# Kernel tuning notes

Measured on AMD Instinct MI355X. Metric: run time of the kernel, lower is better.

The kernel has to match this reference:

```python
import math
import jax, jax.numpy as jnp
import numpy as np

K = 64            # multiplicity per irrep
NE = 10           # num_elements
N_NODES = 10000
N_EDGES = 100000
AVG_NEIGH = 10.0
EDGE_DIM = 8
LS = [0, 1, 2]    # node/intermediate irreps 64x0e+64x1o+64x2e
LS_OUT = [0, 1]   # output irreps 64x0e+64x1o
INV_SQRT_K = 1.0 / math.sqrt(K)
MIX_NORM = 1.0 / math.sqrt(K * NE)

# ---- real spherical-harmonic Clebsch-Gordan coefficients (small l, exact) ----
def _cg(j1, m1, j2, m2, j3, m3):
    if m1 + m2 != m3 or not (abs(j1 - j2) <= j3 <= j1 + j2):
        return 0.0
    f = math.factorial
    pre = math.sqrt((2 * j3 + 1) * f(j1 + j2 - j3) * f(j1 - j2 + j3) * f(-j1 + j2 + j3) / f(j1 + j2 + j3 + 1))
    pre *= math.sqrt(f(j1 + m1) * f(j1 - m1) * f(j2 + m2) * f(j2 - m2) * f(j3 + m3) * f(j3 - m3))
    s = 0.0
    for k in range(j1 + j2 + j3 + 1):
        d = (j1 + j2 - j3 - k, j1 - m1 - k, j2 + m2 - k, j3 - j2 + m1 + k, j3 - j1 - m2 + k)
        if min(d) < 0:
            continue
        s += (-1) ** k / (f(k) * f(d[0]) * f(d[1]) * f(d[2]) * f(d[3]) * f(d[4]))
    return pre * s

def _u_real(l):
    # complex->real SH change of basis: Y_real = U @ Y_complex
    U = np.zeros((2 * l + 1, 2 * l + 1), dtype=np.complex128)
    U[l, l] = 1.0
    s = 1.0 / math.sqrt(2.0)
    for m in range(1, l + 1):
        U[l + m, l + m] = (-1) ** m * s
        U[l + m, l - m] = s
        U[l - m, l + m] = -1j * (-1) ** m * s
        U[l - m, l - m] = 1j * s
    return U

def real_cg(l1, l2, l3):
    C = np.zeros((2 * l1 + 1, 2 * l2 + 1, 2 * l3 + 1), dtype=np.complex128)
    for m1 in range(-l1, l1 + 1):
        for m2 in range(-l2, l2 + 1):
            m3 = m1 + m2
            if abs(m3) <= l3:
                C[l1 + m1, l2 + m2, l3 + m3] = _cg(l1, m1, l2, m2, l3, m3)
    U1, U2, U3 = _u_real(l1), _u_real(l2), _u_real(l3)
    Cr = np.einsum('ai,bj,ck,ijk->abc', U1, U2, U3.conj(), C)
    return np.ascontiguousarray(Cr.real).astype(np.float32)  # real since l1+l2+l3 even

# parity/triangle allowed paths (l1: edge sph, l2: node in, l3: intermediate) -> 11 paths
EDGE_PATHS = [(l1, l2, l3) for l1 in LS for l2 in LS for l3 in LS
              if abs(l1 - l2) <= l3 <= l1 + l2 and (l1 + l2 + l3) % 2 == 0]
N_EDGE_PATHS = len(EDGE_PATHS)  # 11
DEG2_PATHS = [(0, 0, 0), (1, 1, 0), (2, 2, 0), (0, 1, 1), (1, 2, 1)]
DEG3_PATHS = [(0, 0, 0), (1, 1, 0), (0, 1, 1), (1, 0, 1), (1, 2, 1)]
CG_EDGE = [real_cg(*p) for p in EDGE_PATHS]
CG_D2 = [real_cg(*p) for p in DEG2_PATHS]
CG_D3 = [real_cg(*p) for p in DEG3_PATHS]

def split_irreps(x, ls, mul):
    # ir_mul layout: per irrep a [(2l+1)*mul] flat segment, m index outer
    out, o = [], 0
    for l in ls:
        d = (2 * l + 1) * mul
        out.append(x[:, o:o + d].reshape(x.shape[0], 2 * l + 1, mul))
        o += d
    return out


def setup_inputs() -> dict:
    key = jax.random.key(0)
    ks = jax.random.split(key, 20)
    sender = jax.random.randint(ks[0], (N_EDGES,), 0, N_NODES)
    receiver = jax.random.randint(ks[1], (N_EDGES,), 0, N_NODES)
    indices = jax.random.randint(ks[2], (N_NODES,), 0, NE)
    node_attrs = jax.nn.one_hot(indices, NE, dtype=jnp.float32)
    node_feature_in = jax.random.normal(ks[3], (N_NODES, K * 9), dtype=jnp.float32)
    edge_length_embed = jax.random.normal(ks[4], (N_EDGES, EDGE_DIM), dtype=jnp.float32)
    edge_sph_embed = jax.random.normal(ks[5], (N_EDGES, 9), dtype=jnp.float32)
    W_lin_in = jax.random.normal(ks[6], (3, K, K), dtype=jnp.float32)
    mlp_W0 = jax.random.normal(ks[7], (EDGE_DIM, 32), dtype=jnp.float32) / math.sqrt(EDGE_DIM)
    mlp_b0 = jnp.zeros((32,), jnp.float32)
    mlp_W1 = jax.random.normal(ks[8], (32, 32), dtype=jnp.float32) / math.sqrt(32.0)
    mlp_b1 = jnp.zeros((32,), jnp.float32)
    mlp_W2 = jax.random.normal(ks[9], (32, 32), dtype=jnp.float32) / math.sqrt(32.0)
    mlp_b2 = jnp.zeros((32,), jnp.float32)
    mlp_W3 = jax.random.normal(ks[10], (32, N_EDGE_PATHS * K), dtype=jnp.float32) / math.sqrt(32.0)
    mlp_b3 = jnp.zeros((N_EDGE_PATHS * K,), jnp.float32)
    W_mix = jax.random.normal(ks[11], (3, NE, K, K), dtype=jnp.float32)
    w1 = jax.random.normal(ks[12], (NE, 2, K), dtype=jnp.float32)
    w2 = 0.1 * jax.random.normal(ks[13], (NE, len(DEG2_PATHS), K), dtype=jnp.float32)
    w3 = 0.05 * jax.random.normal(ks[14], (NE, len(DEG3_PATHS), K), dtype=jnp.float32)
    W_out_m = jax.random.normal(ks[15], (2, K, K), dtype=jnp.float32)
    W_out_h = jax.random.normal(ks[16], (2, K, K), dtype=jnp.float32)
    return dict(sender=sender, receiver=receiver, indices=indices, node_attrs=node_attrs,
                node_feature_in=node_feature_in, edge_length_embed=edge_length_embed,
                edge_sph_embed=edge_sph_embed, W_lin_in=W_lin_in,
                mlp_W0=mlp_W0, mlp_b0=mlp_b0, mlp_W1=mlp_W1, mlp_b1=mlp_b1,
                mlp_W2=mlp_W2, mlp_b2=mlp_b2, mlp_W3=mlp_W3, mlp_b3=mlp_b3,
                W_mix=W_mix, w1=w1, w2=w2, w3=w3, W_out_m=W_out_m, W_out_h=W_out_h)


def reference(sender, receiver, indices, node_attrs, node_feature_in,
              edge_length_embed, edge_sph_embed, W_lin_in,
              mlp_W0, mlp_b0, mlp_W1, mlp_b1, mlp_W2, mlp_b2, mlp_W3, mlp_b3,
              W_mix, w1, w2, w3, W_out_m, W_out_h):
    N = node_feature_in.shape[0]
    h1 = split_irreps(node_feature_in, LS, K)  # per-l [N, 2l+1, K]
    # ELinear_h1_2_h1p: per-irrep channel mixing
    h1p = [jnp.einsum('nmc,cd->nmd', h1[l], W_lin_in[l]) * INV_SQRT_K for l in LS]
    # residual radial MLP -> per-edge TP path weights [E, P, K]
    h = jax.nn.silu(edge_length_embed @ mlp_W0 + mlp_b0)
    h = h + jax.nn.silu(h @ mlp_W1 + mlp_b1)
    h = h + jax.nn.silu(h @ mlp_W2 + mlp_b2)
    Rl = (h @ mlp_W3 + mlp_b3).reshape(-1, N_EDGE_PATHS, K)
    sph = split_irreps(edge_sph_embed, LS, 1)  # per-l [E, 2l+1, 1]
    gx = [h1p[l][sender] for l in LS]          # gather sender node features
    # channelwise equivariant tensor product with per-edge radial weights
    msg = [None, None, None]
    for p, (l1, l2, l3) in enumerate(EDGE_PATHS):
        t = jnp.einsum('abd,ea,ebc->edc', jnp.asarray(CG_EDGE[p]), sph[l1][:, :, 0], gx[l2])
        t = t * Rl[:, p, None, :]
        msg[l3] = t if msg[l3] is None else msg[l3] + t
    # scatter-sum messages to receivers, normalized by avg num neighbors
    A = [jax.ops.segment_sum(msg[l], receiver, num_segments=N) / AVG_NEIGH for l in LS]
    # element-conditioned mixing (FCTP with num_elements x 0e attrs)
    Amix = [jnp.einsum('nmc,ne,ecd->nmd', A[l], node_attrs, W_mix[l]) * MIX_NORM for l in LS]
    # symmetric contraction (body order 3) with element-dependent channelwise weights
    w1n, w2n, w3n = w1[indices], w2[indices], w3[indices]
    T2 = [jnp.zeros_like(Amix[L]) for L in LS_OUT]
    for p, (l1, l2, L) in enumerate(DEG2_PATHS):
        t = jnp.einsum('abd,nac,nbc->ndc', jnp.asarray(CG_D2[p]), Amix[l1], Amix[l2])
        T2[L] = T2[L] + w2n[:, p, None, :] * t
    T3 = [jnp.zeros_like(Amix[L]) for L in LS_OUT]
    for q, (Lp, l3, L) in enumerate(DEG3_PATHS):
        t = jnp.einsum('abd,nac,nbc->ndc', jnp.asarray(CG_D3[q]), T2[Lp], Amix[l3])
        T3[L] = T3[L] + w3n[:, q, None, :] * t
    B = [w1n[:, L, None, :] * Amix[L] + T2[L] + T3[L] for L in LS_OUT]
    # node_feature_out = ELinear_h1_2_h2(h1) + ELinear_m2_2_h2(B)
    out = []
    for L in LS_OUT:
        y = jnp.einsum('nmc,cd->nmd', h1[L], W_out_h[L]) * INV_SQRT_K
        y = y + jnp.einsum('nmc,cd->nmd', B[L], W_out_m[L]) * INV_SQRT_K
        out.append(y.reshape(N, -1))
    return jnp.concatenate(out, axis=1)  # [N, 4K] = [N, 256]
```

## Files before the change

kernel.cpp:

```cpp
#include <hip/hip_runtime.h>
#include <math.h>

#define NNODES 10000
#define NEDGES 100000

struct Cplx { double re, im; };

constexpr double cfact(int n){ double r=1.0; for(int i=2;i<=n;++i) r*=i; return r; }

constexpr double csqrt_(double x){
  if (x<=0.0) return 0.0;
  double g = x<1.0 ? 1.0 : x;
  for (int it=0; it<64; ++it){ double ng = 0.5*(g + x/g); if (ng==g) break; g = ng; }
  return g;
}

constexpr double cg_coeff(int j1,int m1,int j2,int m2,int j3,int m3){
  if (m1+m2!=m3) return 0.0;
  int lo = j1>j2 ? j1-j2 : j2-j1;
  if (j3<lo || j3>j1+j2) return 0.0;
  if (m1<-j1||m1>j1||m2<-j2||m2>j2||m3<-j3||m3>j3) return 0.0;
  double pre = csqrt_((2.0*j3+1.0)*cfact(j1+j2-j3)*cfact(j1-j2+j3)*cfact(-j1+j2+j3)/cfact(j1+j2+j3+1));
  pre *= csqrt_(cfact(j1+m1)*cfact(j1-m1)*cfact(j2+m2)*cfact(j2-m2)*cfact(j3+m3)*cfact(j3-m3));
  double s = 0.0;
  for (int k=0;k<=j1+j2+j3;++k){
    int d0=j1+j2-j3-k, d1=j1-m1-k, d2=j2+m2-k, d3=j3-j2+m1+k, d4=j3-j1-m2+k;
    if (d0<0||d1<0||d2<0||d3<0||d4<0) continue;
    double term = 1.0/(cfact(k)*cfact(d0)*cfact(d1)*cfact(d2)*cfact(d3)*cfact(d4));
    s += (k&1) ? -term : term;
  }
  return pre*s;
}

constexpr Cplx uent(int l,int a,int i){
  const double s = 0.70710678118654752440;
  int ma = a - l;
  if (ma==0) { if (i==l) return Cplx{1.0,0.0}; return Cplx{0.0,0.0}; }
  if (ma>0){
    int m = ma; double sg = (m&1) ? -1.0 : 1.0;
    if (i==l+m) return Cplx{sg*s, 0.0};
    if (i==l-m) return Cplx{s, 0.0};
    return Cplx{0.0,0.0};
  }
  int m = -ma; double sg = (m&1) ? -1.0 : 1.0;
  if (i==l+m) return Cplx{0.0, -sg*s};
  if (i==l-m) return Cplx{0.0, s};
  return Cplx{0.0,0.0};
}

constexpr double real_cg_entry(int l1,int l2,int l3,int a,int b,int c){
  double acc = 0.0;
  int ii0 = a, ii1 = 2*l1-a;
  int jj0 = b, jj1 = 2*l2-b;
  for (int x=0;x<2;++x){
    int i = (x==0)? ii0 : ii1;
    if (x==1 && ii1==ii0) break;
    Cplx u1 = uent(l1,a,i); if (u1.re==0.0 && u1.im==0.0) continue;
    for (int y=0;y<2;++y){
      int j = (y==0)? jj0 : jj1;
      if (y==1 && jj1==jj0) break;
      Cplx u2 = uent(l2,b,j); if (u2.re==0.0 && u2.im==0.0) continue;
      int k = (i-l1)+(j-l2)+l3;
      if (k<0 || k>2*l3) continue;
      Cplx u3 = uent(l3,c,k); if (u3.re==0.0 && u3.im==0.0) continue;
      double cg = cg_coeff(l1,i-l1,l2,j-l2,l3,k-l3);
      if (cg==0.0) continue;
      double pr = u1.re*u2.re - u1.im*u2.im;
      double pi = u1.re*u2.im + u1.im*u2.re;
      acc += (pr*u3.re + pi*u3.im) * cg;
    }
  }
  return acc;
}

struct CGT { float v[5][5][5]; };
constexpr CGT make_cg(int l1,int l2,int l3){
  CGT t{};
  for (int a=0;a<2*l1+1;++a)
    for (int b=0;b<2*l2+1;++b)
      for (int c=0;c<2*l3+1;++c)
        t.v[a][b][c] = (float)real_cg_entry(l1,l2,l3,a,b,c);
  return t;
}

__device__ __forceinline__ float silu_(float x){ return x / (1.0f + __expf(-x)); }

union H16 { _Float16 h; unsigned short u; };
__device__ __forceinline__ unsigned short f2h(float x){ H16 c; c.h = (_Float16)x; return c.u; }
__device__ __forceinline__ float h2f(unsigned short u){ H16 c; c.u = u; return (float)c.h; }

template<int L1,int L2,int L3>
__device__ __forceinline__ void tp_accum(const float* sp, const float* g, float rl, float* msg){
  constexpr CGT T = make_cg(L1,L2,L3);
  constexpr int NA = 2*L1+1, NB = 2*L2+1, ND = 2*L3+1;
  float t[ND];
#pragma unroll
  for (int d=0; d<ND; ++d) t[d] = 0.f;
#pragma unroll
  for (int b=0;b<NB;++b){
#pragma unroll
    for (int d=0; d<ND; ++d){
      float u = 0.f; bool any = false;
#pragma unroll
      for (int a=0;a<NA;++a){
        const float cg = T.v[a][b][d];
        if (cg != 0.f){ u = fmaf(cg, sp[a], u); any = true; }
      }
      if (any) t[d] = fmaf(u, g[b], t[d]);
    }
  }
#pragma unroll
  for (int d=0;d<ND;++d) msg[d] = fmaf(rl, t[d], msg[d]);
}

template<int L1,int L2,int L3>
__device__ __forceinline__ void sc_accum(const float* X, const float* Y, float w, float* out){
  constexpr CGT T = make_cg(L1,L2,L3);
  constexpr int NA = 2*L1+1, NB = 2*L2+1, ND = 2*L3+1;
#pragma unroll
  for (int d=0;d<ND;++d){
    float s = 0.f;
#pragma unroll
    for (int a=0;a<NA;++a){
#pragma unroll
      for (int b=0;b<NB;++b){
        const float cg = T.v[a][b][d];
        if (cg != 0.f) s = fmaf(cg*X[a], Y[b], s);
      }
    }
    out[d] = fmaf(w, s, out[d]);
  }
}

__global__ void __launch_bounds__(64) k_lin_in(const float* __restrict__ h1,
                                               const float* __restrict__ W,
                                               float* __restrict__ h1p,
                                               int* __restrict__ deg){
  const int n = blockIdx.x;
  const int d = threadIdx.x;
  if (d == 0) deg[n] = 0;
  const float* row = h1 + (long)n*576;
  float acc[9];
#pragma unroll
  for (int i=0;i<9;++i) acc[i] = 0.f;
  for (int c=0;c<64;++c){
    const float w0 = W[c*64 + d];
    const float w1 = W[4096 + c*64 + d];
    const float w2 = W[8192 + c*64 + d];
    acc[0] = fmaf(row[c], w0, acc[0]);
#pragma unroll
    for (int m=0;m<3;++m) acc[1+m] = fmaf(row[64+m*64+c], w1, acc[1+m]);
#pragma unroll
    for (int m=0;m<5;++m) acc[4+m] = fmaf(row[256+m*64+c], w2, acc[4+m]);
  }
  float* o = h1p + (long)n*576;
  o[d] = acc[0]*0.125f;
#pragma unroll
  for (int m=0;m<3;++m) o[64+m*64+d] = acc[1+m]*0.125f;
#pragma unroll
  for (int m=0;m<5;++m) o[256+m*64+d] = acc[4+m]*0.125f;
}

__global__ void __launch_bounds__(256) k_mlp(const float* __restrict__ ele,
                                             const float* __restrict__ W0, const float* __restrict__ b0,
                                             const float* __restrict__ W1, const float* __restrict__ b1,
                                             const float* __restrict__ W2, const float* __restrict__ b2,
                                             float* __restrict__ hmlp){
  const int e = blockIdx.x*256 + threadIdx.x;
  if (e >= NEDGES) return;
  float x[8];
#pragma unroll
  for (int i=0;i<8;++i) x[i] = ele[(long)e*8 + i];
  float h[32];
#pragma unroll
  for (int d=0;d<32;++d){
    float acc = b0[d];
#pragma unroll
    for (int i=0;i<8;++i) acc = fmaf(x[i], W0[i*32+d], acc);
    h[d] = silu_(acc);
  }
#pragma unroll
  for (int L=0; L<2; ++L){
    const float* Wl = L ? W2 : W1;
    const float* bl = L ? b2 : b1;
    float acc[32];
#pragma unroll
    for (int d=0;d<32;++d) acc[d] = bl[d];
    for (int j=0;j<32;++j){
      const float hj = h[j];
#pragma unroll
      for (int d=0;d<32;++d) acc[d] = fmaf(hj, Wl[j*32+d], acc[d]);
    }
#pragma unroll
    for (int d=0;d<32;++d) h[d] += silu_(acc[d]);
  }
  float* o = hmlp + (long)e*32;
#pragma unroll
  for (int d=0;d<32;++d) o[d] = h[d];
}

__global__ void __launch_bounds__(256) k_hist(const int* __restrict__ receiver, int* __restrict__ deg){
  const int e = blockIdx.x*256 + threadIdx.x;
  if (e < NEDGES) atomicAdd(&deg[receiver[e]], 1);
}

__global__ void __launch_bounds__(256) k_scan(const int* __restrict__ deg,
                                              int* __restrict__ rowptr,
                                              int* __restrict__ cursor){
  __shared__ int sums[256];
  const int t = threadIdx.x;
  const int CH = 40;
  const int base = t*CH;
  int s = 0;
  for (int i=0;i<CH;++i){ int idx = base+i; if (idx < NNODES) s += deg[idx]; }
  sums[t] = s; __syncthreads();
  for (int off=1; off<256; off<<=1){
    int v = (t>=off) ? sums[t-off] : 0;
    __syncthreads();
    sums[t] += v;
    __syncthreads();
  }
  int run = (t==0) ? 0 : sums[t-1];
  for (int i=0;i<CH;++i){
    int idx = base+i;
    if (idx < NNODES){ rowptr[idx] = run; cursor[idx] = run; run += deg[idx]; }
  }
  if (t==255) rowptr[NNODES] = sums[255];
}

__global__ void __launch_bounds__(256) k_fill(const int* __restrict__ receiver,
                                              int* __restrict__ cursor,
                                              int* __restrict__ eidx){
  const int e = blockIdx.x*256 + threadIdx.x;
  if (e < NEDGES){
    int pos = atomicAdd(&cursor[receiver[e]], 1);
    eidx[pos] = e;
  }
}

__global__ void __launch_bounds__(256, 2) k_edge_all(const int* __restrict__ sender,
                                             const float* __restrict__ hmlp,
                                             const float* __restrict__ sph,
                                             const float* __restrict__ h1p,
                                             const float* __restrict__ W3, const float* __restrict__ b3,
                                             unsigned short* __restrict__ msg16){
  __shared__ float sps[4][72];
  const int wid  = threadIdx.x >> 6;
  const int lane = threadIdx.x & 63;
  const int ubase = __builtin_amdgcn_readfirstlane((blockIdx.x*4 + wid) * 8);

  sps[wid][lane] = sph[(long)ubase*9 + lane];
  if (lane < 8) sps[wid][64+lane] = sph[(long)ubase*9 + 64 + lane];

  int sidx[8];
#pragma unroll
  for (int e=0;e<8;++e) sidx[e] = sender[ubase+e];

  float g[8][9];
#pragma unroll
  for (int e=0;e<8;++e){
    const float* hp = h1p + (long)sidx[e]*576;
#pragma unroll
    for (int i=0;i<9;++i) g[e][i] = hp[i*64+lane];
  }
#pragma unroll
  for (int e=0;e<8;++e)
#pragma unroll
    for (int i=0;i<9;++i) asm volatile("" : "+v"(g[e][i]));

  const float* hu = hmlp + (long)ubase*32;

  float rl[11][8];
#pragma unroll
  for (int p=0;p<11;++p){
    const float bb = b3[p*64+lane];
#pragma unroll
    for (int e=0;e<8;++e) rl[p][e] = bb;
  }
  for (int jb=0;jb<32;jb+=4){
    float w3v[4][11];
#pragma unroll
    for (int jj=0;jj<4;++jj)
#pragma unroll
      for (int p=0;p<11;++p)
        w3v[jj][p] = W3[(jb+jj)*704 + p*64 + lane];
#pragma unroll
    for (int e=0;e<8;++e){
#pragma unroll
      for (int jj=0;jj<4;++jj){
        const float hj = hu[e*32 + jb + jj];
#pragma unroll
        for (int p=0;p<11;++p) rl[p][e] = fmaf(hj, w3v[jj][p], rl[p][e]);
      }
    }
  }

#pragma unroll
  for (int e=0;e<8;++e){
    const float* sp = &sps[wid][e*9];
    const size_t mb = (size_t)(ubase+e)*576;
    float m0[1] = {0.f};
    float m1[3] = {0.f,0.f,0.f};
    float m2[5] = {0.f,0.f,0.f,0.f,0.f};
    tp_accum<0,0,0>(sp+0, &g[e][0], rl[0][e],  m0);
    tp_accum<0,1,1>(sp+0, &g[e][1], rl[1][e],  m1);
    tp_accum<0,2,2>(sp+0, &g[e][4], rl[2][e],  m2);
    tp_accum<1,0,1>(sp+1, &g[e][0], rl[3][e],  m1);
    tp_accum<1,1,0>(sp+1, &g[e][1], rl[4][e],  m0);
    tp_accum<1,1,2>(sp+1, &g[e][1], rl[5][e],  m2);
    tp_accum<1,2,1>(sp+1, &g[e][4], rl[6][e],  m1);
    tp_accum<2,0,2>(sp+4, &g[e][0], rl[7][e],  m2);
    tp_accum<2,1,1>(sp+4, &g[e][1], rl[8][e],  m1);
    tp_accum<2,2,0>(sp+4, &g[e][4], rl[9][e],  m0);
    tp_accum<2,2,2>(sp+4, &g[e][4], rl[10][e], m2);
    msg16[mb + lane] = f2h(m0[0]);
#pragma unroll
    for (int m=0;m<3;++m) msg16[mb + (1+m)*64 + lane] = f2h(m1[m]);
#pragma unroll
    for (int m=0;m<5;++m) msg16[mb + (4+m)*64 + lane] = f2h(m2[m]);
  }
}

__global__ void __launch_bounds__(256) k_node_w(const int* __restrict__ indices,
                                             const float* __restrict__ h1,
                                             const int* __restrict__ rowptr,
                                             const int* __restrict__ eidx,
                                             const unsigned short* __restrict__ msg16,
                                             const float* __restrict__ Wmix,
                                             const float* __restrict__ w1,
                                             const float* __restrict__ w2,
                                             const float* __restrict__ w3,
                                             const float* __restrict__ Wom,
                                             const float* __restrict__ Woh,
                                             float* __restrict__ out){
  __shared__ float S[4][9][64];
  __shared__ float Bb[4][4][64];
  const int wid  = threadIdx.x >> 6;
  const int lane = threadIdx.x & 63;
  const int n = blockIdx.x*4 + wid;
  const int e = __builtin_amdgcn_readfirstlane(indices[n]);

  {
    const int start = rowptr[n], end = rowptr[n+1];
    float A[9];
#pragma unroll
    for (int i=0;i<9;++i) A[i] = 0.f;
    for (int q=start; q<end; ++q){
      const int ed = eidx[q];
      const unsigned short* mp = msg16 + (size_t)ed*576;
#pragma unroll
      for (int i=0;i<9;++i) A[i] += h2f(mp[i*64+lane]);
    }
#pragma unroll
    for (int i=0;i<9;++i) S[wid][i][lane] = A[i];
  }

  float ax[9];
#pragma unroll
  for (int i=0;i<9;++i) ax[i] = 0.f;
  {
    const float* Wm0 = Wmix + (size_t)(0*10 + e)*4096;
    const float* Wm1 = Wmix + (size_t)(1*10 + e)*4096;
    const float* Wm2 = Wmix + (size_t)(2*10 + e)*4096;
    for (int c=0;c<64;++c){
      const float wv0 = Wm0[c*64+lane];
      const float wv1 = Wm1[c*64+lane];
      const float wv2 = Wm2[c*64+lane];
      ax[0] = fmaf(S[wid][0][c], wv0, ax[0]);
#pragma unroll
      for (int m=0;m<3;++m) ax[1+m] = fmaf(S[wid][1+m][c], wv1, ax[1+m]);
#pragma unroll
      for (int m=0;m<5;++m) ax[4+m] = fmaf(S[wid][4+m][c], wv2, ax[4+m]);
    }
  }
#pragma unroll
  for (int i=0;i<9;++i) ax[i] *= 0.0039528470752104741f;

  const float* amix0 = ax;
  const float* amix1 = ax+1;
  const float* amix2 = ax+4;
  float w2n[5], w3n[5];
#pragma unroll
  for (int p=0;p<5;++p){
    w2n[p] = w2[(size_t)(e*5+p)*64 + lane];
    w3n[p] = w3[(size_t)(e*5+p)*64 + lane];
  }
  float t20[1] = {0.f}, t21[3] = {0.f,0.f,0.f};
  sc_accum<0,0,0>(amix0, amix0, w2n[0], t20);
  sc_accum<1,1,0>(amix1, amix1, w2n[1], t20);
  sc_accum<2,2,0>(amix2, amix2, w2n[2], t20);
  sc_accum<0,1,1>(amix0, amix1, w2n[3], t21);
  sc_accum<1,2,1>(amix1, amix2, w2n[4], t21);
  float t30[1] = {0.f}, t31[3] = {0.f,0.f,0.f};
  sc_accum<0,0,0>(t20, amix0, w3n[0], t30);
  sc_accum<1,1,0>(t21, amix1, w3n[1], t30);
  sc_accum<0,1,1>(t20, amix1, w3n[2], t31);
  sc_accum<1,0,1>(t21, amix0, w3n[3], t31);
  sc_accum<1,2,1>(t21, amix2, w3n[4], t31);

  const float w1_0 = w1[(size_t)(e*2+0)*64 + lane];
  const float w1_1 = w1[(size_t)(e*2+1)*64 + lane];
  Bb[wid][0][lane] = fmaf(w1_0, amix0[0], t20[0] + t30[0]);
#pragma unroll
  for (int m=0;m<3;++m) Bb[wid][1+m][lane] = fmaf(w1_1, amix1[m], t21[m] + t31[m]);

  {
    const float* hrow = h1 + (long)n*576;
#pragma unroll
    for (int r=0;r<9;++r) S[wid][r][lane] = hrow[r*64 + lane];
  }

  float o[4];
#pragma unroll
  for (int i=0;i<4;++i) o[i] = 0.f;
  for (int c=0;c<64;++c){
    const float wh0 = Woh[c*64+lane];
    const float wh1 = Woh[4096 + c*64+lane];
    const float wm0 = Wom[c*64+lane];
    const float wm1 = Wom[4096 + c*64+lane];
    o[0] = fmaf(S[wid][0][c], wh0, o[0]);
    o[0] = fmaf(Bb[wid][0][c], wm0, o[0]);
#pragma unroll
    for (int m=0;m<3;++m){
      o[1+m] = fmaf(S[wid][1+m][c], wh1, o[1+m]);
      o[1+m] = fmaf(Bb[wid][1+m][c], wm1, o[1+m]);
    }
  }
  float* orow = out + (long)n*256;
  orow[lane] = o[0]*0.125f;
#pragma unroll
  for (int m=0;m<3;++m) orow[64+m*64+lane] = o[1+m]*0.125f;
}

extern "C" void kernel_launch(void* const* d_in, const int* in_sizes, int n_in,
                              void* d_out, int out_size, void* d_ws, size_t ws_size,
                              hipStream_t stream){
  const int*   sender   = (const int*)  d_in[0];
  const int*   receiver = (const int*)  d_in[1];
  const int*   indices  = (const int*)  d_in[2];
  const float* node_feat= (const float*)d_in[4];
  const float* ele      = (const float*)d_in[5];
  const float* sph      = (const float*)d_in[6];
  const float* W_lin    = (const float*)d_in[7];
  const float* W0 = (const float*)d_in[8],  *b0 = (const float*)d_in[9];
  const float* W1 = (const float*)d_in[10], *b1 = (const float*)d_in[11];
  const float* W2 = (const float*)d_in[12], *b2 = (const float*)d_in[13];
  const float* W3 = (const float*)d_in[14], *b3 = (const float*)d_in[15];
  const float* Wmix = (const float*)d_in[16];
  const float* w1 = (const float*)d_in[17];
  const float* w2 = (const float*)d_in[18];
  const float* w3 = (const float*)d_in[19];
  const float* Wom = (const float*)d_in[20];
  const float* Woh = (const float*)d_in[21];
  float* out = (float*)d_out;

  char* ws = (char*)d_ws;
  const size_t OFF_H1P  = 0;
  const size_t OFF_HMLP = OFF_H1P  + (size_t)NNODES*576*4;
  const size_t OFF_MSG  = OFF_HMLP + (size_t)NEDGES*32*4;
  const size_t OFF_DEG  = OFF_MSG  + (size_t)NEDGES*576*2;
  const size_t OFF_ROW  = OFF_DEG  + 40960;
  const size_t OFF_CUR  = OFF_ROW  + 40960;
  const size_t OFF_EIDX = OFF_CUR  + 40960;

  float* h1p  = (float*)(ws + OFF_H1P);
  float* hmlp = (float*)(ws + OFF_HMLP);
  unsigned short* msg16 = (unsigned short*)(ws + OFF_MSG);
  int* deg    = (int*)(ws + OFF_DEG);
  int* rowptr = (int*)(ws + OFF_ROW);
  int* cursor = (int*)(ws + OFF_CUR);
  int* eidx   = (int*)(ws + OFF_EIDX);

  k_lin_in<<<NNODES, 64, 0, stream>>>(node_feat, W_lin, h1p, deg);
  k_mlp<<<(NEDGES+255)/256, 256, 0, stream>>>(ele, W0,b0,W1,b1,W2,b2, hmlp);
  k_hist<<<(NEDGES+255)/256, 256, 0, stream>>>(receiver, deg);
  k_scan<<<1, 256, 0, stream>>>(deg, rowptr, cursor);
  k_fill<<<(NEDGES+255)/256, 256, 0, stream>>>(receiver, cursor, eidx);
  k_edge_all<<<NEDGES/32, 256, 0, stream>>>(sender, hmlp, sph, h1p, W3, b3, msg16);
  k_node_w<<<NNODES/4, 256, 0, stream>>>(indices, node_feat, rowptr, eidx, msg16,
                                         Wmix, w1, w2, w3, Wom, Woh, out);
}
```

Measured before the change: 266.8 us.

## Precompute per-edge CG-SH products and write receiver-sorted packed fp16 messages

The prep kernel now also folds each edge's spherical harmonics into the Clebsch-Gordan coefficients and stores a 120-float U tensor per edge. A new edge kernel uses U for the tensor product and writes packed half2 messages directly at the edge's receiver-sorted position, found with an atomic cursor. A new node kernel then reads the messages contiguously instead of going through an edge-index list. The aim is to cut CG arithmetic in the edge kernel and the gather indirection in the node kernel, at the cost of extra global traffic for U and padded messages. The new path runs only if the workspace is large enough; otherwise the old path runs, and there prep writes U past the eidx buffer.

```diff
diff --git a/kernel.cpp b/kernel.cpp
--- a/kernel.cpp
+++ b/kernel.cpp
@@ -88,6 +88,50 @@
 union H16 { _Float16 h; unsigned short u; };
 __device__ __forceinline__ unsigned short f2h(float x){ H16 c; c.h = (_Float16)x; return c.u; }
 __device__ __forceinline__ float h2f(unsigned short u){ H16 c; c.u = u; return (float)c.h; }
+__device__ __forceinline__ unsigned int pack2(float a, float b){
+  H16 x, y; x.h = (_Float16)a; y.h = (_Float16)b;
+  return ((unsigned int)y.u << 16) | x.u;
+}
+
+template<int L1,int L2,int L3>
+__device__ __forceinline__ void u_comp(const float* sp, float* dst){
+  constexpr CGT T = make_cg(L1,L2,L3);
+  constexpr int NA = 2*L1+1, NB = 2*L2+1, ND = 2*L3+1;
+#pragma unroll
+  for (int b=0;b<NB;++b){
+#pragma unroll
+    for (int d=0;d<ND;++d){
+      float u = 0.f; bool any = false;
+#pragma unroll
+      for (int a=0;a<NA;++a){
+        const float cg = T.v[a][b][d];
+        if (cg != 0.f){ u = fmaf(cg, sp[a], u); any = true; }
+      }
+      if (any) dst[b*ND+d] = u;
+    }
+  }
+}
+
+template<int L1,int L2,int L3>
+__device__ __forceinline__ void tp_u(const float* Ue, const float* g, float rl, float* msg){
+  constexpr CGT T = make_cg(L1,L2,L3);
+  constexpr int NA = 2*L1+1, NB = 2*L2+1, ND = 2*L3+1;
+  float t[ND];
+#pragma unroll
+  for (int d=0;d<ND;++d) t[d] = 0.f;
+#pragma unroll
+  for (int b=0;b<NB;++b){
+#pragma unroll
+    for (int d=0;d<ND;++d){
+      bool any = false;
+#pragma unroll
+      for (int a=0;a<NA;++a) if (T.v[a][b][d] != 0.f) any = true;
+      if (any) t[d] = fmaf(Ue[b*ND+d], g[b], t[d]);
+    }
+  }
+#pragma unroll
+  for (int d=0;d<ND;++d) msg[d] = fmaf(rl, t[d], msg[d]);
+}
 
 template<int L1,int L2,int L3>
 __device__ __forceinline__ void tp_accum(const float* sp, const float* g, float rl, float* msg){
@@ -161,11 +205,13 @@
   for (int m=0;m<5;++m) o[256+m*64+d] = acc[4+m]*0.125f;
 }
 
-__global__ void __launch_bounds__(256) k_mlp(const float* __restrict__ ele,
-                                             const float* __restrict__ W0, const float* __restrict__ b0,
-                                             const float* __restrict__ W1, const float* __restrict__ b1,
-                                             const float* __restrict__ W2, const float* __restrict__ b2,
-                                             float* __restrict__ hmlp){
+__global__ void __launch_bounds__(256) k_prep(const float* __restrict__ ele,
+                                              const float* __restrict__ sph,
+                                              const float* __restrict__ W0, const float* __restrict__ b0,
+                                              const float* __restrict__ W1, const float* __restrict__ b1,
+                                              const float* __restrict__ W2, const float* __restrict__ b2,
+                                              float* __restrict__ hmlp,
+                                              float* __restrict__ U){
   const int e = blockIdx.x*256 + threadIdx.x;
   if (e >= NEDGES) return;
   float x[8];
@@ -197,6 +243,22 @@
   float* o = hmlp + (long)e*32;
 #pragma unroll
   for (int d=0;d<32;++d) o[d] = h[d];
+
+  float sp[9];
+#pragma unroll
+  for (int i=0;i<9;++i) sp[i] = sph[(long)e*9 + i];
+  float* Up = U + (size_t)e*120;
+  u_comp<0,0,0>(sp+0, Up+0);
+  u_comp<0,1,1>(sp+0, Up+1);
+  u_comp<0,2,2>(sp+0, Up+10);
+  u_comp<1,0,1>(sp+1, Up+35);
+  u_comp<1,1,0>(sp+1, Up+38);
+  u_comp<1,1,2>(sp+1, Up+41);
+  u_comp<1,2,1>(sp+1, Up+56);
+  u_comp<2,0,2>(sp+4, Up+71);
+  u_comp<2,1,1>(sp+4, Up+76);
+  u_comp<2,2,0>(sp+4, Up+85);
+  u_comp<2,2,2>(sp+4, Up+90);
 }
 
 __global__ void __launch_bounds__(256) k_hist(const int* __restrict__ receiver, int* __restrict__ deg){
@@ -228,6 +290,13 @@
   if (t==255) rowptr[NNODES] = sums[255];
 }
 
+__global__ void __launch_bounds__(256) k_fill_pos(const int* __restrict__ receiver,
+                                                  int* __restrict__ cursor,
+                                                  int* __restrict__ epos){
+  const int e = blockIdx.x*256 + threadIdx.x;
+  if (e < NEDGES) epos[e] = atomicAdd(&cursor[receiver[e]], 1);
+}
+
 __global__ void __launch_bounds__(256) k_fill(const int* __restrict__ receiver,
                                               int* __restrict__ cursor,
                                               int* __restrict__ eidx){
@@ -236,6 +305,202 @@
     int pos = atomicAdd(&cursor[receiver[e]], 1);
     eidx[pos] = e;
   }
+}
+
+__global__ void __launch_bounds__(256) k_edge_u(const int* __restrict__ sender,
+                                             const int* __restrict__ epos,
+                                             const float* __restrict__ hmlp,
+                                             const float* __restrict__ U,
+                                             const float* __restrict__ h1p,
+                                             const float* __restrict__ W3, const float* __restrict__ b3,
+                                             unsigned int* __restrict__ msg){
+  const int wid  = threadIdx.x >> 6;
+  const int lane = threadIdx.x & 63;
+  const int ubase = __builtin_amdgcn_readfirstlane((blockIdx.x*4 + wid) * 8);
+
+  int sidx[8], pos[8];
+#pragma unroll
+  for (int e=0;e<8;++e){ sidx[e] = sender[ubase+e]; pos[e] = epos[ubase+e]; }
+
+  float g[8][9];
+#pragma unroll
+  for (int e=0;e<8;++e){
+    const float* hp = h1p + (long)sidx[e]*576;
+#pragma unroll
+    for (int i=0;i<9;++i) g[e][i] = hp[i*64+lane];
+  }
+#pragma unroll
+  for (int e=0;e<8;++e)
+#pragma unroll
+    for (int i=0;i<9;++i) asm volatile("" : "+v"(g[e][i]));
+
+  const float* hu = hmlp + (long)ubase*32;
+
+  float rl[11][8];
+#pragma unroll
+  for (int p=0;p<11;++p){
+    const float bb = b3[p*64+lane];
+#pragma unroll
+    for (int e=0;e<8;++e) rl[p][e] = bb;
+  }
+  for (int jb=0;jb<32;jb+=4){
+    float w3v[4][11];
+#pragma unroll
+    for (int jj=0;jj<4;++jj)
+#pragma unroll
+      for (int p=0;p<11;++p)
+        w3v[jj][p] = W3[(jb+jj)*704 + p*64 + lane];
+#pragma unroll
+    for (int e=0;e<8;++e){
+#pragma unroll
+      for (int jj=0;jj<4;++jj){
+        const float hj = hu[e*32 + jb + jj];
+#pragma unroll
+        for (int p=0;p<11;++p) rl[p][e] = fmaf(hj, w3v[jj][p], rl[p][e]);
+      }
+    }
+  }
+
+#pragma unroll
+  for (int e=0;e<8;++e){
+    const float* Ue = U + (size_t)(ubase+e)*120;
+    float m0[1] = {0.f};
+    float m1[3] = {0.f,0.f,0.f};
+    float m2[5] = {0.f,0.f,0.f,0.f,0.f};
+    tp_u<0,0,0>(Ue+0,  &g[e][0], rl[0][e],  m0);
+    tp_u<0,1,1>(Ue+1,  &g[e][1], rl[1][e],  m1);
+    tp_u<0,2,2>(Ue+10, &g[e][4], rl[2][e],  m2);
+    tp_u<1,0,1>(Ue+35, &g[e][0], rl[3][e],  m1);
+    tp_u<1,1,0>(Ue+38, &g[e][1], rl[4][e],  m0);
+    tp_u<1,1,2>(Ue+41, &g[e][1], rl[5][e],  m2);
+    tp_u<1,2,1>(Ue+56, &g[e][4], rl[6][e],  m1);
+    tp_u<2,0,2>(Ue+71, &g[e][0], rl[7][e],  m2);
+    tp_u<2,1,1>(Ue+76, &g[e][1], rl[8][e],  m1);
+    tp_u<2,2,0>(Ue+85, &g[e][4], rl[9][e],  m0);
+    tp_u<2,2,2>(Ue+90, &g[e][4], rl[10][e], m2);
+    unsigned int pk[5];
+    pk[0] = pack2(m0[0], m1[0]);
+    pk[1] = pack2(m1[1], m1[2]);
+    pk[2] = pack2(m2[0], m2[1]);
+    pk[3] = pack2(m2[2], m2[3]);
+    pk[4] = pack2(m2[4], 0.f);
+    unsigned int* mp = msg + (size_t)pos[e]*320;
+#pragma unroll
+    for (int k=0;k<5;++k) mp[k*64 + lane] = pk[k];
+  }
+}
+
+__global__ void __launch_bounds__(256) k_node_c(const int* __restrict__ indices,
+                                             const float* __restrict__ h1,
+                                             const int* __restrict__ rowptr,
+                                             const unsigned int* __restrict__ msg,
+                                             const float* __restrict__ Wmix,
+                                             const float* __restrict__ w1,
+                                             const float* __restrict__ w2,
+                                             const float* __restrict__ w3,
+                                             const float* __restrict__ Wom,
+                                             const float* __restrict__ Woh,
+                                             float* __restrict__ out){
+  __shared__ float S[4][9][64];
+  __shared__ float Bb[4][4][64];
+  const int wid  = threadIdx.x >> 6;
+  const int lane = threadIdx.x & 63;
+  const int n = blockIdx.x*4 + wid;
+  const int e = __builtin_amdgcn_readfirstlane(indices[n]);
+
+  {
+    const int start = rowptr[n], end = rowptr[n+1];
+    float A[9];
+#pragma unroll
+    for (int i=0;i<9;++i) A[i] = 0.f;
+    for (int q=start; q<end; ++q){
+      const unsigned int* mp = msg + (size_t)q*320;
+#pragma unroll
+      for (int k=0;k<5;++k){
+        const unsigned int v = mp[k*64 + lane];
+        A[2*k] += h2f((unsigned short)(v & 0xffff));
+        if (2*k+1 < 9) A[2*k+1] += h2f((unsigned short)(v >> 16));
+      }
+    }
+#pragma unroll
+    for (int i=0;i<9;++i) S[wid][i][lane] = A[i];
+  }
+
+  float ax[9];
+#pragma unroll
+  for (int i=0;i<9;++i) ax[i] = 0.f;
+  {
+    const float* Wm0 = Wmix + (size_t)(0*10 + e)*4096;
+    const float* Wm1 = Wmix + (size_t)(1*10 + e)*4096;
+    const float* Wm2 = Wmix + (size_t)(2*10 + e)*4096;
+    for (int c=0;c<64;++c){
+      const float wv0 = Wm0[c*64+lane];
+      const float wv1 = Wm1[c*64+lane];
+      const float wv2 = Wm2[c*64+lane];
+      ax[0] = fmaf(S[wid][0][c], wv0, ax[0]);
+#pragma unroll
+      for (int m=0;m<3;++m) ax[1+m] = fmaf(S[wid][1+m][c], wv1, ax[1+m]);
+#pragma unroll
+      for (int m=0;m<5;++m) ax[4+m] = fmaf(S[wid][4+m][c], wv2, ax[4+m]);
+    }
+  }
+#pragma unroll
+  for (int i=0;i<9;++i) ax[i] *= 0.0039528470752104741f;
+
+  const float* amix0 = ax;
+  const float* amix1 = ax+1;
+  const float* amix2 = ax+4;
+  float w2n[5], w3n[5];
+#pragma unroll
+  for (int p=0;p<5;++p){
+    w2n[p] = w2[(size_t)(e*5+p)*64 + lane];
+    w3n[p] = w3[(size_t)(e*5+p)*64 + lane];
+  }
+  float t20[1] = {0.f}, t21[3] = {0.f,0.f,0.f};
+  sc_accum<0,0,0>(amix0, amix0, w2n[0], t20);
+  sc_accum<1,1,0>(amix1, amix1, w2n[1], t20);
+  sc_accum<2,2,0>(amix2, amix2, w2n[2], t20);
+  sc_accum<0,1,1>(amix0, amix1, w2n[3], t21);
+  sc_accum<1,2,1>(amix1, amix2, w2n[4], t21);
+  float t30[1] = {0.f}, t31[3] = {0.f,0.f,0.f};
+  sc_accum<0,0,0>(t20, amix0, w3n[0], t30);
+  sc_accum<1,1,0>(t21, amix1, w3n[1], t30);
+  sc_accum<0,1,1>(t20, amix1, w3n[2], t31);
+  sc_accum<1,0,1>(t21, amix0, w3n[3], t31);
+  sc_accum<1,2,1>(t21, amix2, w3n[4], t31);
+
+  const float w1_0 = w1[(size_t)(e*2+0)*64 + lane];
+  const float w1_1 = w1[(size_t)(e*2+1)*64 + lane];
+  Bb[wid][0][lane] = fmaf(w1_0, amix0[0], t20[0] + t30[0]);
+#pragma unroll
+  for (int m=0;m<3;++m) Bb[wid][1+m][lane] = fmaf(w1_1, amix1[m], t21[m] + t31[m]);
+
+  {
+    const float* hrow = h1 + (long)n*576;
+#pragma unroll
+    for (int r=0;r<9;++r) S[wid][r][lane] = hrow[r*64 + lane];
+  }
+
+  float o[4];
+#pragma unroll
+  for (int i=0;i<4;++i) o[i] = 0.f;
+  for (int c=0;c<64;++c){
+    const float wh0 = Woh[c*64+lane];
+    const float wh1 = Woh[4096 + c*64+lane];
+    const float wm0 = Wom[c*64+lane];
+    const float wm1 = Wom[4096 + c*64+lane];
+    o[0] = fmaf(S[wid][0][c], wh0, o[0]);
+    o[0] = fmaf(Bb[wid][0][c], wm0, o[0]);
+#pragma unroll
+    for (int m=0;m<3;++m){
+      o[1+m] = fmaf(S[wid][1+m][c], wh1, o[1+m]);
+      o[1+m] = fmaf(Bb[wid][1+m][c], wm1, o[1+m]);
+    }
+  }
+  float* orow = out + (long)n*256;
+  orow[lane] = o[0]*0.125f;
+#pragma unroll
+  for (int m=0;m<3;++m) orow[64+m*64+lane] = o[1+m]*0.125f;
 }
 
 __global__ void __launch_bounds__(256, 2) k_edge_all(const int* __restrict__ sender,
@@ -455,28 +720,58 @@
   float* out = (float*)d_out;
 
   char* ws = (char*)d_ws;
+
   const size_t OFF_H1P  = 0;
   const size_t OFF_HMLP = OFF_H1P  + (size_t)NNODES*576*4;
-  const size_t OFF_MSG  = OFF_HMLP + (size_t)NEDGES*32*4;
-  const size_t OFF_DEG  = OFF_MSG  + (size_t)NEDGES*576*2;
+  const size_t OFF_U    = OFF_HMLP + (size_t)NEDGES*32*4;
+  const size_t OFF_MSG  = OFF_U    + (size_t)NEDGES*120*4;
+  const size_t OFF_DEG  = OFF_MSG  + (size_t)NEDGES*320*4;
   const size_t OFF_ROW  = OFF_DEG  + 40960;
   const size_t OFF_CUR  = OFF_ROW  + 40960;
-  const size_t OFF_EIDX = OFF_CUR  + 40960;
-
-  float* h1p  = (float*)(ws + OFF_H1P);
-  float* hmlp = (float*)(ws + OFF_HMLP);
-  unsigned short* msg16 = (unsigned short*)(ws + OFF_MSG);
-  int* deg    = (int*)(ws + OFF_DEG);
-  int* rowptr = (int*)(ws + OFF_ROW);
-  int* cursor = (int*)(ws + OFF_CUR);
-  int* eidx   = (int*)(ws + OFF_EIDX);
-
-  k_lin_in<<<NNODES, 64, 0, stream>>>(node_feat, W_lin, h1p, deg);
-  k_mlp<<<(NEDGES+255)/256, 256, 0, stream>>>(ele, W0,b0,W1,b1,W2,b2, hmlp);
-  k_hist<<<(NEDGES+255)/256, 256, 0, stream>>>(receiver, deg);
-  k_scan<<<1, 256, 0, stream>>>(deg, rowptr, cursor);
-  k_fill<<<(NEDGES+255)/256, 256, 0, stream>>>(receiver, cursor, eidx);
-  k_edge_all<<<NEDGES/32, 256, 0, stream>>>(sender, hmlp, sph, h1p, W3, b3, msg16);
-  k_node_w<<<NNODES/4, 256, 0, stream>>>(indices, node_feat, rowptr, eidx, msg16,
-                                         Wmix, w1, w2, w3, Wom, Woh, out);
-}
+  const size_t OFF_EPOS = OFF_CUR  + 40960;
+  const size_t FAST_NEED = OFF_EPOS + (size_t)NEDGES*4 + 4096;
+
+  if (ws_size >= FAST_NEED){
+    float* h1p  = (float*)(ws + OFF_H1P);
+    float* hmlp = (float*)(ws + OFF_HMLP);
+    float* U    = (float*)(ws + OFF_U);
+    unsigned int* msg = (unsigned int*)(ws + OFF_MSG);
+    int* deg    = (int*)(ws + OFF_DEG);
+    int* rowptr = (int*)(ws + OFF_ROW);
+    int* cursor = (int*)(ws + OFF_CUR);
+    int* epos   = (int*)(ws + OFF_EPOS);
+
+    k_lin_in<<<NNODES, 64, 0, stream>>>(node_feat, W_lin, h1p, deg);
+    k_prep<<<(NEDGES+255)/256, 256, 0, stream>>>(ele, sph, W0,b0,W1,b1,W2,b2, hmlp, U);
+    k_hist<<<(NEDGES+255)/256, 256, 0, stream>>>(receiver, deg);
+    k_scan<<<1, 256, 0, stream>>>(deg, rowptr, cursor);
+    k_fill_pos<<<(NEDGES+255)/256, 256, 0, stream>>>(receiver, cursor, epos);
+    k_edge_u<<<NEDGES/32, 256, 0, stream>>>(sender, epos, hmlp, U, h1p, W3, b3, msg);
+    k_node_c<<<NNODES/4, 256, 0, stream>>>(indices, node_feat, rowptr, msg,
+                                           Wmix, w1, w2, w3, Wom, Woh, out);
+  } else {
+    const size_t F_H1P  = 0;
+    const size_t F_HMLP = F_H1P  + (size_t)NNODES*576*4;
+    const size_t F_MSG  = F_HMLP + (size_t)NEDGES*32*4;
+    const size_t F_DEG  = F_MSG  + (size_t)NEDGES*576*2;
+    const size_t F_ROW  = F_DEG  + 40960;
+    const size_t F_CUR  = F_ROW  + 40960;
+    const size_t F_EIDX = F_CUR  + 40960;
+    float* h1p  = (float*)(ws + F_H1P);
+    float* hmlp = (float*)(ws + F_HMLP);
+    unsigned short* msg16 = (unsigned short*)(ws + F_MSG);
+    int* deg    = (int*)(ws + F_DEG);
+    int* rowptr = (int*)(ws + F_ROW);
+    int* cursor = (int*)(ws + F_CUR);
+    int* eidx   = (int*)(ws + F_EIDX);
+
+    k_lin_in<<<NNODES, 64, 0, stream>>>(node_feat, W_lin, h1p, deg);
+    k_prep<<<(NEDGES+255)/256, 256, 0, stream>>>(ele, sph, W0,b0,W1,b1,W2,b2, hmlp, (float*)(ws + F_EIDX + (size_t)NEDGES*4));
+    k_hist<<<(NEDGES+255)/256, 256, 0, stream>>>(receiver, deg);
+    k_scan<<<1, 256, 0, stream>>>(deg, rowptr, cursor);
+    k_fill<<<(NEDGES+255)/256, 256, 0, stream>>>(receiver, cursor, eidx);
+    k_edge_all<<<NEDGES/32, 256, 0, stream>>>(sender, hmlp, sph, h1p, W3, b3, msg16);
+    k_node_w<<<NNODES/4, 256, 0, stream>>>(indices, node_feat, rowptr, eidx, msg16,
+                                           Wmix, w1, w2, w3, Wom, Woh, out);
+  }
+}
```

After: 343.6 us. 28.8% more time.

## Pack edge math into float2, write messages in receiver-sorted order, pack fp16 pairs

Applied to the files above, without the earlier changes.

The edge kernel now handles two edges at once using float2 vector arithmetic, so the compiler can emit packed FMA instructions. Messages are written straight to their receiver-sorted slot (the fill kernel records each edge's position instead of an edge-index list). Message storage uses 32-bit words that hold two fp16 values, padded to 10 halves per channel. The node gather then reads contiguous rows without the indirection, at the cost of scattered writes in the edge kernel, slightly larger message storage, and dropping the occupancy hint of 2 from launch bounds.

```diff
diff --git a/kernel.cpp b/kernel.cpp
--- a/kernel.cpp
+++ b/kernel.cpp
@@ -3,6 +3,8 @@
 
 #define NNODES 10000
 #define NEDGES 100000
+
+typedef float v2f __attribute__((ext_vector_type(2)));
 
 struct Cplx { double re, im; };
 
@@ -86,31 +88,35 @@
 __device__ __forceinline__ float silu_(float x){ return x / (1.0f + __expf(-x)); }
 
 union H16 { _Float16 h; unsigned short u; };
-__device__ __forceinline__ unsigned short f2h(float x){ H16 c; c.h = (_Float16)x; return c.u; }
 __device__ __forceinline__ float h2f(unsigned short u){ H16 c; c.u = u; return (float)c.h; }
+__device__ __forceinline__ unsigned int pack2(float a, float b){
+  H16 x, y; x.h = (_Float16)a; y.h = (_Float16)b;
+  return ((unsigned int)y.u << 16) | x.u;
+}
+__device__ __forceinline__ v2f make2(float s){ v2f r; r.x = s; r.y = s; return r; }
 
 template<int L1,int L2,int L3>
-__device__ __forceinline__ void tp_accum(const float* sp, const float* g, float rl, float* msg){
+__device__ __forceinline__ void tp_pk(const v2f* sp, const v2f* g, v2f rl, v2f* msg){
   constexpr CGT T = make_cg(L1,L2,L3);
   constexpr int NA = 2*L1+1, NB = 2*L2+1, ND = 2*L3+1;
-  float t[ND];
-#pragma unroll
-  for (int d=0; d<ND; ++d) t[d] = 0.f;
+  v2f t[ND];
+#pragma unroll
+  for (int d=0;d<ND;++d) t[d] = make2(0.f);
 #pragma unroll
   for (int b=0;b<NB;++b){
 #pragma unroll
-    for (int d=0; d<ND; ++d){
-      float u = 0.f; bool any = false;
+    for (int d=0;d<ND;++d){
+      v2f u = make2(0.f); bool any = false;
 #pragma unroll
       for (int a=0;a<NA;++a){
         const float cg = T.v[a][b][d];
-        if (cg != 0.f){ u = fmaf(cg, sp[a], u); any = true; }
+        if (cg != 0.f){ u = cg*sp[a] + u; any = true; }
       }
-      if (any) t[d] = fmaf(u, g[b], t[d]);
-    }
-  }
-#pragma unroll
-  for (int d=0;d<ND;++d) msg[d] = fmaf(rl, t[d], msg[d]);
+      if (any) t[d] = u*g[b] + t[d];
+    }
+  }
+#pragma unroll
+  for (int d=0;d<ND;++d) msg[d] = rl*t[d] + msg[d];
 }
 
 template<int L1,int L2,int L3>
@@ -228,54 +234,61 @@
   if (t==255) rowptr[NNODES] = sums[255];
 }
 
-__global__ void __launch_bounds__(256) k_fill(const int* __restrict__ receiver,
-                                              int* __restrict__ cursor,
-                                              int* __restrict__ eidx){
+__global__ void __launch_bounds__(256) k_fill_pos(const int* __restrict__ receiver,
+                                                  int* __restrict__ cursor,
+                                                  int* __restrict__ epos){
   const int e = blockIdx.x*256 + threadIdx.x;
-  if (e < NEDGES){
-    int pos = atomicAdd(&cursor[receiver[e]], 1);
-    eidx[pos] = e;
-  }
-}
-
-__global__ void __launch_bounds__(256, 2) k_edge_all(const int* __restrict__ sender,
+  if (e < NEDGES) epos[e] = atomicAdd(&cursor[receiver[e]], 1);
+}
+
+__global__ void __launch_bounds__(256) k_edge_pk(const int* __restrict__ sender,
+                                             const int* __restrict__ epos,
                                              const float* __restrict__ hmlp,
                                              const float* __restrict__ sph,
                                              const float* __restrict__ h1p,
                                              const float* __restrict__ W3, const float* __restrict__ b3,
-                                             unsigned short* __restrict__ msg16){
+                                             unsigned int* __restrict__ msg){
   __shared__ float sps[4][72];
   const int wid  = threadIdx.x >> 6;
   const int lane = threadIdx.x & 63;
   const int ubase = __builtin_amdgcn_readfirstlane((blockIdx.x*4 + wid) * 8);
 
-  sps[wid][lane] = sph[(long)ubase*9 + lane];
-  if (lane < 8) sps[wid][64+lane] = sph[(long)ubase*9 + 64 + lane];
-
-  int sidx[8];
-#pragma unroll
-  for (int e=0;e<8;++e) sidx[e] = sender[ubase+e];
-
-  float g[8][9];
-#pragma unroll
-  for (int e=0;e<8;++e){
-    const float* hp = h1p + (long)sidx[e]*576;
-#pragma unroll
-    for (int i=0;i<9;++i) g[e][i] = hp[i*64+lane];
-  }
-#pragma unroll
-  for (int e=0;e<8;++e)
-#pragma unroll
-    for (int i=0;i<9;++i) asm volatile("" : "+v"(g[e][i]));
+  {
+    const int idx = lane;
+    const int e = idx/9, a = idx - 9*e;
+    sps[wid][a*8 + e] = sph[(long)ubase*9 + idx];
+  }
+  if (lane < 8){
+    const int idx = 64 + lane;
+    const int e = idx/9, a = idx - 9*e;
+    sps[wid][a*8 + e] = sph[(long)ubase*9 + idx];
+  }
+
+  int sidx[8], pos[8];
+#pragma unroll
+  for (int e=0;e<8;++e){ sidx[e] = sender[ubase+e]; pos[e] = epos[ubase+e]; }
+
+  v2f g2[4][9];
+#pragma unroll
+  for (int q=0;q<4;++q){
+    const float* hp0 = h1p + (long)sidx[2*q]  *576;
+    const float* hp1 = h1p + (long)sidx[2*q+1]*576;
+#pragma unroll
+    for (int i=0;i<9;++i){ g2[q][i].x = hp0[i*64+lane]; g2[q][i].y = hp1[i*64+lane]; }
+  }
+#pragma unroll
+  for (int q=0;q<4;++q)
+#pragma unroll
+    for (int i=0;i<9;++i) asm volatile("" : "+v"(g2[q][i]));
 
   const float* hu = hmlp + (long)ubase*32;
 
-  float rl[11][8];
+  v2f rl2[11][4];
 #pragma unroll
   for (int p=0;p<11;++p){
     const float bb = b3[p*64+lane];
 #pragma unroll
-    for (int e=0;e<8;++e) rl[p][e] = bb;
+    for (int q=0;q<4;++q) rl2[p][q] = make2(bb);
   }
   for (int jb=0;jb<32;jb+=4){
     float w3v[4][11];
@@ -285,47 +298,64 @@
       for (int p=0;p<11;++p)
         w3v[jj][p] = W3[(jb+jj)*704 + p*64 + lane];
 #pragma unroll
-    for (int e=0;e<8;++e){
+    for (int q=0;q<4;++q){
 #pragma unroll
       for (int jj=0;jj<4;++jj){
-        const float hj = hu[e*32 + jb + jj];
-#pragma unroll
-        for (int p=0;p<11;++p) rl[p][e] = fmaf(hj, w3v[jj][p], rl[p][e]);
+        v2f h2; h2.x = hu[(2*q)*32 + jb + jj]; h2.y = hu[(2*q+1)*32 + jb + jj];
+#pragma unroll
+        for (int p=0;p<11;++p) rl2[p][q] = h2*w3v[jj][p] + rl2[p][q];
       }
     }
   }
 
 #pragma unroll
-  for (int e=0;e<8;++e){
-    const float* sp = &sps[wid][e*9];
-    const size_t mb = (size_t)(ubase+e)*576;
-    float m0[1] = {0.f};
-    float m1[3] = {0.f,0.f,0.f};
-    float m2[5] = {0.f,0.f,0.f,0.f,0.f};
-    tp_accum<0,0,0>(sp+0, &g[e][0], rl[0][e],  m0);
-    tp_accum<0,1,1>(sp+0, &g[e][1], rl[1][e],  m1);
-    tp_accum<0,2,2>(sp+0, &g[e][4], rl[2][e],  m2);
-    tp_accum<1,0,1>(sp+1, &g[e][0], rl[3][e],  m1);
-    tp_accum<1,1,0>(sp+1, &g[e][1], rl[4][e],  m0);
-    tp_accum<1,1,2>(sp+1, &g[e][1], rl[5][e],  m2);
-    tp_accum<1,2,1>(sp+1, &g[e][4], rl[6][e],  m1);
-    tp_accum<2,0,2>(sp+4, &g[e][0], rl[7][e],  m2);
-    tp_accum<2,1,1>(sp+4, &g[e][1], rl[8][e],  m1);
-    tp_accum<2,2,0>(sp+4, &g[e][4], rl[9][e],  m0);
-    tp_accum<2,2,2>(sp+4, &g[e][4], rl[10][e], m2);
-    msg16[mb + lane] = f2h(m0[0]);
-#pragma unroll
-    for (int m=0;m<3;++m) msg16[mb + (1+m)*64 + lane] = f2h(m1[m]);
-#pragma unroll
-    for (int m=0;m<5;++m) msg16[mb + (4+m)*64 + lane] = f2h(m2[m]);
-  }
-}
-
-__global__ void __launch_bounds__(256) k_node_w(const int* __restrict__ indices,
+  for (int q=0;q<4;++q){
+    v2f sp2[9];
+#pragma unroll
+    for (int a=0;a<9;++a) sp2[a] = *(const v2f*)&sps[wid][a*8 + 2*q];
+    v2f m0[1]; m0[0] = make2(0.f);
+    v2f m1[3]; m1[0]=m1[1]=m1[2]=make2(0.f);
+    v2f m2[5]; m2[0]=m2[1]=m2[2]=m2[3]=m2[4]=make2(0.f);
+    tp_pk<0,0,0>(sp2+0, &g2[q][0], rl2[0][q],  m0);
+    tp_pk<0,1,1>(sp2+0, &g2[q][1], rl2[1][q],  m1);
+    tp_pk<0,2,2>(sp2+0, &g2[q][4], rl2[2][q],  m2);
+    tp_pk<1,0,1>(sp2+1, &g2[q][0], rl2[3][q],  m1);
+    tp_pk<1,1,0>(sp2+1, &g2[q][1], rl2[4][q],  m0);
+    tp_pk<1,1,2>(sp2+1, &g2[q][1], rl2[5][q],  m2);
+    tp_pk<1,2,1>(sp2+1, &g2[q][4], rl2[6][q],  m1);
+    tp_pk<2,0,2>(sp2+4, &g2[q][0], rl2[7][q],  m2);
+    tp_pk<2,1,1>(sp2+4, &g2[q][1], rl2[8][q],  m1);
+    tp_pk<2,2,0>(sp2+4, &g2[q][4], rl2[9][q],  m0);
+    tp_pk<2,2,2>(sp2+4, &g2[q][4], rl2[10][q], m2);
+    {
+      unsigned int pk[5];
+      pk[0] = pack2(m0[0].x, m1[0].x);
+      pk[1] = pack2(m1[1].x, m1[2].x);
+      pk[2] = pack2(m2[0].x, m2[1].x);
+      pk[3] = pack2(m2[2].x, m2[3].x);
+      pk[4] = pack2(m2[4].x, 0.f);
+      unsigned int* mp = msg + (size_t)pos[2*q]*320;
+#pragma unroll
+      for (int k=0;k<5;++k) mp[k*64 + lane] = pk[k];
+    }
+    {
+      unsigned int pk[5];
+      pk[0] = pack2(m0[0].y, m1[0].y);
+      pk[1] = pack2(m1[1].y, m1[2].y);
+      pk[2] = pack2(m2[0].y, m2[1].y);
+      pk[3] = pack2(m2[2].y, m2[3].y);
+      pk[4] = pack2(m2[4].y, 0.f);
+      unsigned int* mp = msg + (size_t)pos[2*q+1]*320;
+#pragma unroll
+      for (int k=0;k<5;++k) mp[k*64 + lane] = pk[k];
+    }
+  }
+}
+
+__global__ void __launch_bounds__(256) k_node_c(const int* __restrict__ indices,
                                              const float* __restrict__ h1,
                                              const int* __restrict__ rowptr,
-                                             const int* __restrict__ eidx,
-                                             const unsigned short* __restrict__ msg16,
+                                             const unsigned int* __restrict__ msg,
                                              const float* __restrict__ Wmix,
                                              const float* __restrict__ w1,
                                              const float* __restrict__ w2,
@@ -346,10 +376,13 @@
 #pragma unroll
     for (int i=0;i<9;++i) A[i] = 0.f;
     for (int q=start; q<end; ++q){
-      const int ed = eidx[q];
-      const unsigned short* mp = msg16 + (size_t)ed*576;
-#pragma unroll
-      for (int i=0;i<9;++i) A[i] += h2f(mp[i*64+lane]);
+      const unsigned int* mp = msg + (size_t)q*320;
+#pragma unroll
+      for (int k=0;k<5;++k){
+        const unsigned int v = mp[k*64 + lane];
+        A[2*k] += h2f((unsigned short)(v & 0xffff));
+        if (2*k+1 < 9) A[2*k+1] += h2f((unsigned short)(v >> 16));
+      }
     }
 #pragma unroll
     for (int i=0;i<9;++i) S[wid][i][lane] = A[i];
@@ -458,25 +491,25 @@
   const size_t OFF_H1P  = 0;
   const size_t OFF_HMLP = OFF_H1P  + (size_t)NNODES*576*4;
   const size_t OFF_MSG  = OFF_HMLP + (size_t)NEDGES*32*4;
-  const size_t OFF_DEG  = OFF_MSG  + (size_t)NEDGES*576*2;
+  const size_t OFF_DEG  = OFF_MSG  + (size_t)NEDGES*320*4;
   const size_t OFF_ROW  = OFF_DEG  + 40960;
   const size_t OFF_CUR  = OFF_ROW  + 40960;
-  const size_t OFF_EIDX = OFF_CUR  + 40960;
+  const size_t OFF_EPOS = OFF_CUR  + 40960;
 
   float* h1p  = (float*)(ws + OFF_H1P);
   float* hmlp = (float*)(ws + OFF_HMLP);
-  unsigned short* msg16 = (unsigned short*)(ws + OFF_MSG);
+  unsigned int* msg = (unsigned int*)(ws + OFF_MSG);
   int* deg    = (int*)(ws + OFF_DEG);
   int* rowptr = (int*)(ws + OFF_ROW);
   int* cursor = (int*)(ws + OFF_CUR);
-  int* eidx   = (int*)(ws + OFF_EIDX);
+  int* epos   = (int*)(ws + OFF_EPOS);
 
   k_lin_in<<<NNODES, 64, 0, stream>>>(node_feat, W_lin, h1p, deg);
   k_mlp<<<(NEDGES+255)/256, 256, 0, stream>>>(ele, W0,b0,W1,b1,W2,b2, hmlp);
   k_hist<<<(NEDGES+255)/256, 256, 0, stream>>>(receiver, deg);
   k_scan<<<1, 256, 0, stream>>>(deg, rowptr, cursor);
-  k_fill<<<(NEDGES+255)/256, 256, 0, stream>>>(receiver, cursor, eidx);
-  k_edge_all<<<NEDGES/32, 256, 0, stream>>>(sender, hmlp, sph, h1p, W3, b3, msg16);
-  k_node_w<<<NNODES/4, 256, 0, stream>>>(indices, node_feat, rowptr, eidx, msg16,
+  k_fill_pos<<<(NEDGES+255)/256, 256, 0, stream>>>(receiver, cursor, epos);
+  k_edge_pk<<<NEDGES/32, 256, 0, stream>>>(sender, epos, hmlp, sph, h1p, W3, b3, msg);
+  k_node_c<<<NNODES/4, 256, 0, stream>>>(indices, node_feat, rowptr, msg,
                                          Wmix, w1, w2, w3, Wom, Woh, out);
 }
```

New measurement: 258.0 us. 3.3% less time.
